# Performance work log

Measured on AMD Instinct MI355X. Metric: run time of the kernel, lower is better.

## Reference

```python
import jax, jax.numpy as jnp
from jax import lax
import numpy as np

B, S, I, H, L, D = 64, 1024, 512, 512, 2, 2  # batch, seq, input, hidden, layers, directions


def setup_inputs() -> dict:
    key = jax.random.key(0)
    ks = jax.random.split(key, 6)
    scale = 0.05  # keep gates out of saturation (torch code uses raw randn; scaled for numerics)
    return {
        "x": jax.random.normal(ks[0], (B, S, I), jnp.float32),
        "Wi": jax.random.normal(ks[1], (L, D, 3, I, H), jnp.float32) * scale,  # gates: [r, z, n]
        "Wh": jax.random.normal(ks[2], (L, D, 3, H, H), jnp.float32) * scale,
        "b": jax.random.normal(ks[3], (L, D, 3, H), jnp.float32) * scale,
        "fc_w": jax.random.normal(ks[4], (D * H, H), jnp.float32) * scale,
        "fc_b": jax.random.normal(ks[5], (H,), jnp.float32) * scale,
    }


def _run_layer(x_seq, wi, wh, bb):
    """One GRU layer, one direction. x_seq: [B,S,Hin]; wi/wh: [3,Hin,H]; bb: [3,H]."""
    batch = x_seq.shape[0]
    h_dim = wh.shape[-1]
    # Precompute all input projections (+biases) once: [S, 3, B, H]
    xs = jnp.einsum('bsi,gih->sgbh', x_seq, wi) + bb[None, :, None, :]

    def step(h, xg):
        r = jax.nn.sigmoid(xg[0] + h @ wh[0])
        z = jax.nn.sigmoid(xg[1] + h @ wh[1])
        n = jnp.tanh(xg[2] + r * (h @ wh[2]))
        h_next = (1.0 - z) * n + z * h
        return h_next, h_next

    h0 = jnp.zeros((batch, h_dim), x_seq.dtype)
    _, ys = lax.scan(step, h0, xs)  # ys: [S, B, H]
    return ys.transpose(1, 0, 2)  # [B, S, H]


def reference(x, Wi, Wh, b, fc_w, fc_b):
    n_layers = Wi.shape[0]
    # forward direction: stack layers, feed layer output as next layer input
    out_f = x
    for l in range(n_layers):
        out_f = _run_layer(out_f, Wi[l, 0], Wh[l, 0], b[l, 0])
    # backward direction: process time-reversed sequence, then flip back
    out_b = x[:, ::-1, :]
    for l in range(n_layers):
        out_b = _run_layer(out_b, Wi[l, 1], Wh[l, 1], b[l, 1])
    out_b = out_b[:, ::-1, :]
    outputs = jnp.concatenate([out_f, out_b], axis=2)  # [B, S, 2H]
    return outputs[:, -1, :] @ fc_w + fc_b  # [B, H]
```

## Files before the change

kernel.cpp:

```cpp
#include <hip/hip_runtime.h>
#include <cstdint>
#include <cmath>


typedef __attribute__((ext_vector_type(8))) short bf16x8;
typedef __attribute__((ext_vector_type(4))) float f32x4;
typedef __attribute__((ext_vector_type(4))) unsigned int u32x4;

#define DEV static __device__ __forceinline__

DEV unsigned short f2bf(float f) {
  union { float f; uint32_t u; } v; v.f = f;
  uint32_t u = v.u;
  return (unsigned short)((u + (((u >> 16) & 1u) + 0x7fffu)) >> 16);
}
DEV float bf2f(unsigned short h) {
  union { uint32_t u; float f; } v; v.u = ((uint32_t)h) << 16;
  return v.f;
}
DEV float fsig(float x)  { return 1.f / (1.f + __expf(-x)); }
DEV float ftanh(float x) { return 2.f / (1.f + __expf(-2.f * x)) - 1.f; }

static constexpr int Ss = 1024, Ii = 512;

static constexpr size_t WIMG_PER_LS = 131072;
static constexpr size_t OFF_WIMG = 0;
static constexpr size_t WIMG_BYTES = (size_t)64 * WIMG_PER_LS;
static constexpr size_t OFF_H1  = OFF_WIMG + WIMG_BYTES;
static constexpr size_t OFF_H2  = OFF_H1 + 524288;
static constexpr size_t OFF_FLG = OFF_H2 + 524288;
static constexpr size_t OFF_H2F = OFF_FLG + 1024;
static constexpr size_t OFF_HB1 = OFF_H2F + 131072;
static constexpr size_t OFF_HB2 = OFF_HB1 + 131072;
static constexpr size_t WS_NEED = OFF_HB2 + 131072;

__global__ __launch_bounds__(256) void prep_weights(const float* __restrict__ Wi,
                                                    const float* __restrict__ Wh,
                                                    unsigned short* __restrict__ img) {
  uint32_t idx = blockIdx.x * 256 + threadIdx.x;
  uint32_t ls = idx >> 16;
  uint32_t off = idx & 65535u;
  int l = (int)(ls >> 5), s = (int)(ls & 31);
  int m, g, cc, kg, kr;
  bool lo = off >= 49152u;
  if (!lo) {
    m = (int)(off / 24576u); uint32_t r = off % 24576u;
    kg = (int)(r / 384u); r %= 384u;
    int c = (int)(r >> 3); kr = (int)(r & 7u);
    g = c >> 4; cc = c & 15;
  } else {
    uint32_t o2 = off - 49152u;
    m = (int)(o2 >> 13); uint32_t r = o2 & 8191u;
    kg = (int)(r >> 7); r &= 127u;
    cc = (int)(r >> 3); kr = (int)(r & 7u);
    g = 2;
  }
  int h = s * 16 + cc, k = kg * 8 + kr;
  const float* W = m ? Wh : Wi;
  float v = W[((size_t)(l * 6 + g) * 512 + k) * 512 + h];
  unsigned short hv = f2bf(v);
  if (lo) hv = f2bf(v - bf2f(hv));
  img[(size_t)ls * 65536 + off] = hv;
}

__global__ __launch_bounds__(256) void init_state(uint32_t* __restrict__ hz,
                                                  int* __restrict__ flg) {
  int tid = blockIdx.x * 256 + threadIdx.x;
  if (tid < 262144) hz[tid] = 0u;
  if (tid < 64) flg[tid] = (tid >= 32) ? 1 : 0;
}

#define MFMA(AA, BB, CC) CC = __builtin_amdgcn_mfma_f32_16x16x32_bf16(AA, BB, CC, 0, 0, 0)

#define WAIT2(TA, TB)                                                              \
  {                                                                                \
    const int tgt_ = (lane < 32) ? (TA) : (TB);                                    \
    int spins_ = 0;                                                                \
    for (;;) {                                                                     \
      int v_ = __hip_atomic_load(pollp, __ATOMIC_RELAXED, __HIP_MEMORY_SCOPE_AGENT); \
      if (__all(v_ >= tgt_)) break;                                                \
      __builtin_amdgcn_s_sleep(1);                                                 \
      if (++spins_ > (1 << 20)) {                                                  \
        __hip_atomic_fetch_max((int*)pollp, 0x40000000, __ATOMIC_RELAXED,          \
                               __HIP_MEMORY_SCOPE_AGENT);                          \
        break;                                                                     \
      }                                                                            \
    }                                                                              \
    __builtin_amdgcn_fence(__ATOMIC_ACQUIRE, "agent");                             \
  }

__global__ __launch_bounds__(256, 1) void gru_persistent(const float* __restrict__ x,
                                                         const float* __restrict__ bias,
                                                         unsigned char* __restrict__ ws) {
  __shared__ unsigned char lds[131072];
  const int tid = threadIdx.x, lane = tid & 63, wv = tid >> 6;
  const int bid = blockIdx.x;
  const int layer = bid >> 5, slice = bid & 31;
  const int l15 = lane & 15, q = lane >> 4;

  {
    const u32x4* src = (const u32x4*)(ws + OFF_WIMG + (size_t)(layer * 32 + slice) * WIMG_PER_LS);
    u32x4* dst = (u32x4*)lds;
    for (int i = tid; i < 8192; i += 256) dst[i] = src[i];
  }
  __syncthreads();

  bf16x8 hB[48];
#pragma unroll
  for (int kk = 0; kk < 16; ++kk) {
    const int kg = kk * 4 + q;
    const unsigned char* wb = lds + 49152 + (size_t)kg * 768 + (size_t)l15 * 16;
    hB[kk * 3 + 0] = *(const bf16x8*)(wb);
    hB[kk * 3 + 1] = *(const bf16x8*)(wb + 256);
    hB[kk * 3 + 2] = *(const bf16x8*)(wb + 512);
  }

  unsigned short* h1 = (unsigned short*)(ws + OFF_H1);
  unsigned short* h2 = (unsigned short*)(ws + OFF_H2);
  int* flg = (int*)(ws + OFF_FLG);
  float* h2f = (float*)(ws + OFF_H2F);

  const int colg = slice * 16 + l15;
  const int row0 = wv * 16 + q * 4;
  const float b0 = bias[(size_t)(layer * 6 + 0) * 512 + colg];
  const float b1 = bias[(size_t)(layer * 6 + 1) * 512 + colg];
  const float b2 = bias[(size_t)(layer * 6 + 2) * 512 + colg];

  int* myflag = flg + layer * 32 + slice;
  const int* pollp = flg + lane;
  f32x4 hprev{0.f, 0.f, 0.f, 0.f};

  if (layer == 0) {
    const float* xr0 = x + (size_t)(wv * 16 + l15) * Ss * Ii;
    for (int T = 1; T <= 1024; ++T) {
      f32x4 ax0{}, ax1{}, ax2{}, ah0{}, ah1{}, ah2{};
      const float* xr = xr0 + (size_t)(T - 1) * Ii;
#pragma unroll 4
      for (int kk = 0; kk < 16; ++kk) {
        const int kg = kk * 4 + q;
        f32x4 va = *(const f32x4*)(xr + kg * 8);
        f32x4 vb = *(const f32x4*)(xr + kg * 8 + 4);
        bf16x8 ahi, alo;
#pragma unroll
        for (int e = 0; e < 4; ++e) {
          unsigned short ha = f2bf(va[e]);
          ((unsigned short*)&ahi)[e] = ha;
          ((unsigned short*)&alo)[e] = f2bf(va[e] - bf2f(ha));
          unsigned short hb_ = f2bf(vb[e]);
          ((unsigned short*)&ahi)[e + 4] = hb_;
          ((unsigned short*)&alo)[e + 4] = f2bf(vb[e] - bf2f(hb_));
        }
        const unsigned char* wb = lds + (size_t)kg * 768 + (size_t)l15 * 16;
        bf16x8 q0 = *(const bf16x8*)(wb);
        bf16x8 q1 = *(const bf16x8*)(wb + 256);
        bf16x8 q2 = *(const bf16x8*)(wb + 512);
        bf16x8 ql = *(const bf16x8*)(lds + 98304 + (size_t)kg * 256 + (size_t)l15 * 16);
        MFMA(ahi, q0, ax0); MFMA(alo, q0, ax0);
        MFMA(ahi, q1, ax1); MFMA(alo, q1, ax1);
        MFMA(ahi, q2, ax2); MFMA(alo, q2, ax2);
        MFMA(ahi, ql, ax2);
      }
      WAIT2(T - 1, T - 3);
      const unsigned short* hsrc = h1 + (size_t)((T - 1) & 3) * 65536 + (size_t)(wv * 16 + l15) * 512;
#pragma unroll
      for (int kk = 0; kk < 16; ++kk) {
        const int kg = kk * 4 + q;
        bf16x8 ahi = *(const bf16x8*)(hsrc + kg * 8);
        bf16x8 alo = *(const bf16x8*)(hsrc + 32768 + kg * 8);
        bf16x8 ql = *(const bf16x8*)(lds + 98304 + 16384 + (size_t)kg * 256 + (size_t)l15 * 16);
        MFMA(ahi, hB[kk * 3 + 0], ah0); MFMA(alo, hB[kk * 3 + 0], ah0);
        MFMA(ahi, hB[kk * 3 + 1], ah1); MFMA(alo, hB[kk * 3 + 1], ah1);
        MFMA(ahi, hB[kk * 3 + 2], ah2); MFMA(alo, hB[kk * 3 + 2], ah2);
        MFMA(ahi, ql, ah2);
      }
      unsigned short* hd = h1 + (size_t)(T & 3) * 65536;
#pragma unroll
      for (int e = 0; e < 4; ++e) {
        float rr = fsig(ax0[e] + ah0[e] + b0);
        float zz = fsig(ax1[e] + ah1[e] + b1);
        float nn = ftanh(ax2[e] + b2 + rr * ah2[e]);
        float hn = (1.f - zz) * nn + zz * hprev[e];
        hprev[e] = hn;
        unsigned short hi = f2bf(hn), lo = f2bf(hn - bf2f(hi));
        size_t o = (size_t)(row0 + e) * 512 + colg;
        hd[o] = hi; hd[o + 32768] = lo;
      }
      __syncthreads();
      if (tid == 0)
        __hip_atomic_fetch_max(myflag, T, __ATOMIC_RELEASE, __HIP_MEMORY_SCOPE_AGENT);
    }
  } else {
    for (int T = 2; T <= 1025; ++T) {
      WAIT2(T - 1, T - 1);
      f32x4 ax0{}, ax1{}, ax2{}, ah0{}, ah1{}, ah2{};
      const unsigned short* as = h1 + (size_t)((T - 1) & 3) * 65536 + (size_t)(wv * 16 + l15) * 512;
      const unsigned short* hsrc = h2 + (size_t)((T - 2) & 3) * 65536 + (size_t)(wv * 16 + l15) * 512;
#pragma unroll 4
      for (int kk = 0; kk < 16; ++kk) {
        const int kg = kk * 4 + q;
        bf16x8 ahi = *(const bf16x8*)(as + kg * 8);
        bf16x8 alo = *(const bf16x8*)(as + 32768 + kg * 8);
        const unsigned char* wb = lds + (size_t)kg * 768 + (size_t)l15 * 16;
        bf16x8 q0 = *(const bf16x8*)(wb);
        bf16x8 q1 = *(const bf16x8*)(wb + 256);
        bf16x8 q2 = *(const bf16x8*)(wb + 512);
        bf16x8 ql = *(const bf16x8*)(lds + 98304 + (size_t)kg * 256 + (size_t)l15 * 16);
        MFMA(ahi, q0, ax0); MFMA(alo, q0, ax0);
        MFMA(ahi, q1, ax1); MFMA(alo, q1, ax1);
        MFMA(ahi, q2, ax2); MFMA(alo, q2, ax2);
        MFMA(ahi, ql, ax2);
      }
#pragma unroll
      for (int kk = 0; kk < 16; ++kk) {
        const int kg = kk * 4 + q;
        bf16x8 ahi = *(const bf16x8*)(hsrc + kg * 8);
        bf16x8 alo = *(const bf16x8*)(hsrc + 32768 + kg * 8);
        bf16x8 ql = *(const bf16x8*)(lds + 98304 + 16384 + (size_t)kg * 256 + (size_t)l15 * 16);
        MFMA(ahi, hB[kk * 3 + 0], ah0); MFMA(alo, hB[kk * 3 + 0], ah0);
        MFMA(ahi, hB[kk * 3 + 1], ah1); MFMA(alo, hB[kk * 3 + 1], ah1);
        MFMA(ahi, hB[kk * 3 + 2], ah2); MFMA(alo, hB[kk * 3 + 2], ah2);
        MFMA(ahi, ql, ah2);
      }
      unsigned short* hd = h2 + (size_t)((T - 1) & 3) * 65536;
#pragma unroll
      for (int e = 0; e < 4; ++e) {
        float rr = fsig(ax0[e] + ah0[e] + b0);
        float zz = fsig(ax1[e] + ah1[e] + b1);
        float nn = ftanh(ax2[e] + b2 + rr * ah2[e]);
        float hn = (1.f - zz) * nn + zz * hprev[e];
        hprev[e] = hn;
        unsigned short hi = f2bf(hn), lo = f2bf(hn - bf2f(hi));
        size_t o = (size_t)(row0 + e) * 512 + colg;
        hd[o] = hi; hd[o + 32768] = lo;
        if (T == 1025) h2f[o] = hn;
      }
      __syncthreads();
      if (tid == 0)
        __hip_atomic_fetch_max(myflag, T, __ATOMIC_RELEASE, __HIP_MEMORY_SCOPE_AGENT);
    }
  }
}

__global__ __launch_bounds__(256) void gru_bstep(const float* __restrict__ inp, long rstride,
                                                 const float* __restrict__ Wi,
                                                 const float* __restrict__ bias,
                                                 float* __restrict__ out) {
  __shared__ float a[8192];
  int tid = threadIdx.x;
  int bg = blockIdx.x >> 4, cg = blockIdx.x & 15;
  for (int j = 0; j < 32; ++j) {
    int idx = j * 256 + tid;
    int r = idx >> 9, k = idx & 511;
    a[idx] = inp[(size_t)(bg * 16 + r) * rstride + k];
  }
  __syncthreads();
  int col = cg * 32 + (tid & 31);
  int r0 = tid >> 5;
  float z0 = bias[512 + col], z1 = z0;
  float n0 = bias[1024 + col], n1 = n0;
  const float* W1 = Wi + (size_t)512 * 512;
  const float* W2 = Wi + (size_t)2 * 512 * 512;
  for (int k = 0; k < 512; ++k) {
    float wz = W1[(size_t)k * 512 + col];
    float wn = W2[(size_t)k * 512 + col];
    float a0 = a[r0 * 512 + k], a1 = a[(r0 + 8) * 512 + k];
    z0 += a0 * wz; z1 += a1 * wz;
    n0 += a0 * wn; n1 += a1 * wn;
  }
  float s0 = fsig(z0), s1 = fsig(z1);
  out[(size_t)(bg * 16 + r0) * 512 + col]     = (1.f - s0) * ftanh(n0);
  out[(size_t)(bg * 16 + r0 + 8) * 512 + col] = (1.f - s1) * ftanh(n1);
}

__global__ __launch_bounds__(256) void fc_kernel(const float* __restrict__ h2f,
                                                 const float* __restrict__ hb2,
                                                 const float* __restrict__ fcw,
                                                 const float* __restrict__ fcb,
                                                 float* __restrict__ out) {
  __shared__ float a[16384];
  int tid = threadIdx.x;
  int bg = blockIdx.x >> 4, cg = blockIdx.x & 15;
  for (int j = 0; j < 32; ++j) {
    int idx = j * 256 + tid;
    int r = idx >> 9, k = idx & 511;
    a[r * 1024 + k]       = h2f[(size_t)(bg * 16 + r) * 512 + k];
    a[r * 1024 + 512 + k] = hb2[(size_t)(bg * 16 + r) * 512 + k];
  }
  __syncthreads();
  int col = cg * 32 + (tid & 31);
  int r0 = tid >> 5;
  float s0 = fcb[col], s1 = fcb[col];
  for (int k = 0; k < 1024; ++k) {
    float wvv = fcw[(size_t)k * 512 + col];
    s0 += a[r0 * 1024 + k] * wvv;
    s1 += a[(r0 + 8) * 1024 + k] * wvv;
  }
  out[(size_t)(bg * 16 + r0) * 512 + col]     = s0;
  out[(size_t)(bg * 16 + r0 + 8) * 512 + col] = s1;
}

extern "C" void kernel_launch(void* const* d_in, const int* in_sizes, int n_in,
                              void* d_out, int out_size, void* d_ws, size_t ws_size,
                              hipStream_t stream) {
  const float* x   = (const float*)d_in[0];
  const float* Wi  = (const float*)d_in[1];
  const float* Wh  = (const float*)d_in[2];
  const float* b   = (const float*)d_in[3];
  const float* fcw = (const float*)d_in[4];
  const float* fcb = (const float*)d_in[5];
  float* out = (float*)d_out;
  unsigned char* ws = (unsigned char*)d_ws;
  if (ws_size < WS_NEED) return;

  prep_weights<<<16384, 256, 0, stream>>>(Wi, Wh, (unsigned short*)(ws + OFF_WIMG));
  init_state<<<1024, 256, 0, stream>>>((uint32_t*)(ws + OFF_H1), (int*)(ws + OFF_FLG));
  gru_persistent<<<64, 256, 0, stream>>>(x, b, ws);
  gru_bstep<<<64, 256, 0, stream>>>(x + (size_t)1023 * 512, (long)Ss * Ii,
                                    Wi + (size_t)3 * 512 * 512, b + 3 * 512,
                                    (float*)(ws + OFF_HB1));
  gru_bstep<<<64, 256, 0, stream>>>((const float*)(ws + OFF_HB1), 512L,
                                    Wi + (size_t)9 * 512 * 512, b + 9 * 512,
                                    (float*)(ws + OFF_HB2));
  fc_kernel<<<64, 256, 0, stream>>>((const float*)(ws + OFF_H2F), (const float*)(ws + OFF_HB2),
                                    fcw, fcb, out);
}
```

Measured before the change: 15.37 ms.

## Replace acquire/release flag sync with relaxed atomics and split per-layer waits

The inter-block handshake now uses relaxed agent-scope atomic loads and stores for the h state buffers and an explicit vmcnt wait, in place of acquire fences and release flag updates. This avoids cache invalidation and writeback costs on each step. Waits are split per producer group, so layer 1 can start its own recurrent matmul before layer 0's output is ready, and layer 0 checks the consumer's progress before starting its input projection. The correctness of the relaxed ordering depends on the atomic accesses bypassing non-coherent caches, which is a memory-model risk.

```diff
diff --git a/kernel.cpp b/kernel.cpp
--- a/kernel.cpp
+++ b/kernel.cpp
@@ -72,22 +72,30 @@
 
 #define MFMA(AA, BB, CC) CC = __builtin_amdgcn_mfma_f32_16x16x32_bf16(AA, BB, CC, 0, 0, 0)
 
-#define WAIT2(TA, TB)                                                              \
-  {                                                                                \
-    const int tgt_ = (lane < 32) ? (TA) : (TB);                                    \
-    int spins_ = 0;                                                                \
-    for (;;) {                                                                     \
-      int v_ = __hip_atomic_load(pollp, __ATOMIC_RELAXED, __HIP_MEMORY_SCOPE_AGENT); \
-      if (__all(v_ >= tgt_)) break;                                                \
-      __builtin_amdgcn_s_sleep(1);                                                 \
-      if (++spins_ > (1 << 20)) {                                                  \
-        __hip_atomic_fetch_max((int*)pollp, 0x40000000, __ATOMIC_RELAXED,          \
-                               __HIP_MEMORY_SCOPE_AGENT);                          \
-        break;                                                                     \
-      }                                                                            \
-    }                                                                              \
-    __builtin_amdgcn_fence(__ATOMIC_ACQUIRE, "agent");                             \
-  }
+DEV bf16x8 ldc16(const unsigned short* p) {
+  union { unsigned long long q[2]; bf16x8 v; } u;
+  u.q[0] = __hip_atomic_load((const unsigned long long*)p,       __ATOMIC_RELAXED, __HIP_MEMORY_SCOPE_AGENT);
+  u.q[1] = __hip_atomic_load((const unsigned long long*)(p + 4), __ATOMIC_RELAXED, __HIP_MEMORY_SCOPE_AGENT);
+  return u.v;
+}
+DEV void stc16(unsigned short* p, unsigned short v) {
+  __hip_atomic_store(p, v, __ATOMIC_RELAXED, __HIP_MEMORY_SCOPE_AGENT);
+}
+
+DEV void waitflag(int* flg, int grp, int tgt, int lane) {
+  int* p = flg + grp * 32 + (lane & 31);
+  int spins = 0;
+  for (;;) {
+    int v = __hip_atomic_load(p, __ATOMIC_RELAXED, __HIP_MEMORY_SCOPE_AGENT);
+    if (__all(v >= tgt)) break;
+    __builtin_amdgcn_s_sleep(2);
+    if (++spins > (1 << 19)) {
+      __hip_atomic_fetch_max(p, 0x40000000, __ATOMIC_RELAXED, __HIP_MEMORY_SCOPE_AGENT);
+      break;
+    }
+  }
+  asm volatile("" ::: "memory");
+}
 
 __global__ __launch_bounds__(256, 1) void gru_persistent(const float* __restrict__ x,
                                                          const float* __restrict__ bias,
@@ -127,12 +135,12 @@
   const float b2 = bias[(size_t)(layer * 6 + 2) * 512 + colg];
 
   int* myflag = flg + layer * 32 + slice;
-  const int* pollp = flg + lane;
   f32x4 hprev{0.f, 0.f, 0.f, 0.f};
 
   if (layer == 0) {
     const float* xr0 = x + (size_t)(wv * 16 + l15) * Ss * Ii;
     for (int T = 1; T <= 1024; ++T) {
+      waitflag(flg, 1, T - 3, lane);
       f32x4 ax0{}, ax1{}, ax2{}, ah0{}, ah1{}, ah2{};
       const float* xr = xr0 + (size_t)(T - 1) * Ii;
 #pragma unroll 4
@@ -160,13 +168,13 @@
         MFMA(ahi, q2, ax2); MFMA(alo, q2, ax2);
         MFMA(ahi, ql, ax2);
       }
-      WAIT2(T - 1, T - 3);
+      waitflag(flg, 0, T - 1, lane);
       const unsigned short* hsrc = h1 + (size_t)((T - 1) & 3) * 65536 + (size_t)(wv * 16 + l15) * 512;
 #pragma unroll
       for (int kk = 0; kk < 16; ++kk) {
         const int kg = kk * 4 + q;
-        bf16x8 ahi = *(const bf16x8*)(hsrc + kg * 8);
-        bf16x8 alo = *(const bf16x8*)(hsrc + 32768 + kg * 8);
+        bf16x8 ahi = ldc16(hsrc + kg * 8);
+        bf16x8 alo = ldc16(hsrc + 32768 + kg * 8);
         bf16x8 ql = *(const bf16x8*)(lds + 98304 + 16384 + (size_t)kg * 256 + (size_t)l15 * 16);
         MFMA(ahi, hB[kk * 3 + 0], ah0); MFMA(alo, hB[kk * 3 + 0], ah0);
         MFMA(ahi, hB[kk * 3 + 1], ah1); MFMA(alo, hB[kk * 3 + 1], ah1);
@@ -183,23 +191,36 @@
         hprev[e] = hn;
         unsigned short hi = f2bf(hn), lo = f2bf(hn - bf2f(hi));
         size_t o = (size_t)(row0 + e) * 512 + colg;
-        hd[o] = hi; hd[o + 32768] = lo;
-      }
+        stc16(hd + o, hi); stc16(hd + o + 32768, lo);
+      }
+      asm volatile("s_waitcnt vmcnt(0)" ::: "memory");
       __syncthreads();
       if (tid == 0)
-        __hip_atomic_fetch_max(myflag, T, __ATOMIC_RELEASE, __HIP_MEMORY_SCOPE_AGENT);
+        __hip_atomic_fetch_max(myflag, T, __ATOMIC_RELAXED, __HIP_MEMORY_SCOPE_AGENT);
     }
   } else {
     for (int T = 2; T <= 1025; ++T) {
-      WAIT2(T - 1, T - 1);
       f32x4 ax0{}, ax1{}, ax2{}, ah0{}, ah1{}, ah2{};
+      waitflag(flg, 1, T - 1, lane);
+      const unsigned short* hsrc = h2 + (size_t)((T - 2) & 3) * 65536 + (size_t)(wv * 16 + l15) * 512;
+#pragma unroll
+      for (int kk = 0; kk < 16; ++kk) {
+        const int kg = kk * 4 + q;
+        bf16x8 ahi = ldc16(hsrc + kg * 8);
+        bf16x8 alo = ldc16(hsrc + 32768 + kg * 8);
+        bf16x8 ql = *(const bf16x8*)(lds + 98304 + 16384 + (size_t)kg * 256 + (size_t)l15 * 16);
+        MFMA(ahi, hB[kk * 3 + 0], ah0); MFMA(alo, hB[kk * 3 + 0], ah0);
+        MFMA(ahi, hB[kk * 3 + 1], ah1); MFMA(alo, hB[kk * 3 + 1], ah1);
+        MFMA(ahi, hB[kk * 3 + 2], ah2); MFMA(alo, hB[kk * 3 + 2], ah2);
+        MFMA(ahi, ql, ah2);
+      }
+      waitflag(flg, 0, T - 1, lane);
       const unsigned short* as = h1 + (size_t)((T - 1) & 3) * 65536 + (size_t)(wv * 16 + l15) * 512;
-      const unsigned short* hsrc = h2 + (size_t)((T - 2) & 3) * 65536 + (size_t)(wv * 16 + l15) * 512;
 #pragma unroll 4
       for (int kk = 0; kk < 16; ++kk) {
         const int kg = kk * 4 + q;
-        bf16x8 ahi = *(const bf16x8*)(as + kg * 8);
-        bf16x8 alo = *(const bf16x8*)(as + 32768 + kg * 8);
+        bf16x8 ahi = ldc16(as + kg * 8);
+        bf16x8 alo = ldc16(as + 32768 + kg * 8);
         const unsigned char* wb = lds + (size_t)kg * 768 + (size_t)l15 * 16;
         bf16x8 q0 = *(const bf16x8*)(wb);
         bf16x8 q1 = *(const bf16x8*)(wb + 256);
@@ -210,17 +231,6 @@
         MFMA(ahi, q2, ax2); MFMA(alo, q2, ax2);
         MFMA(ahi, ql, ax2);
       }
-#pragma unroll
-      for (int kk = 0; kk < 16; ++kk) {
-        const int kg = kk * 4 + q;
-        bf16x8 ahi = *(const bf16x8*)(hsrc + kg * 8);
-        bf16x8 alo = *(const bf16x8*)(hsrc + 32768 + kg * 8);
-        bf16x8 ql = *(const bf16x8*)(lds + 98304 + 16384 + (size_t)kg * 256 + (size_t)l15 * 16);
-        MFMA(ahi, hB[kk * 3 + 0], ah0); MFMA(alo, hB[kk * 3 + 0], ah0);
-        MFMA(ahi, hB[kk * 3 + 1], ah1); MFMA(alo, hB[kk * 3 + 1], ah1);
-        MFMA(ahi, hB[kk * 3 + 2], ah2); MFMA(alo, hB[kk * 3 + 2], ah2);
-        MFMA(ahi, ql, ah2);
-      }
       unsigned short* hd = h2 + (size_t)((T - 1) & 3) * 65536;
 #pragma unroll
       for (int e = 0; e < 4; ++e) {
@@ -231,12 +241,13 @@
         hprev[e] = hn;
         unsigned short hi = f2bf(hn), lo = f2bf(hn - bf2f(hi));
         size_t o = (size_t)(row0 + e) * 512 + colg;
-        hd[o] = hi; hd[o + 32768] = lo;
+        stc16(hd + o, hi); stc16(hd + o + 32768, lo);
         if (T == 1025) h2f[o] = hn;
       }
+      asm volatile("s_waitcnt vmcnt(0)" ::: "memory");
       __syncthreads();
       if (tid == 0)
-        __hip_atomic_fetch_max(myflag, T, __ATOMIC_RELEASE, __HIP_MEMORY_SCOPE_AGENT);
+        __hip_atomic_fetch_max(myflag, T, __ATOMIC_RELAXED, __HIP_MEMORY_SCOPE_AGENT);
     }
   }
 }
```

Result: slower. 17.11 ms (+11.4%).

## Pad sync flags, map layers to XCDs, poll with one wave

Applied to the files above, without the earlier changes.

Each per-block progress flag now sits on its own 64-byte line (stride 16 ints) to avoid false sharing. Blocks are remapped so that each layer's slices land on particular XCDs (bid&7), keeping producer and consumer traffic local. Only wave 0 spins on the flags, with a longer sleep, and a __syncthreads releases the other waves. In layer 1 the recurrent h2 matmul is reordered ahead of the h1 input matmul. The trade-off is an extra block barrier per step and coarser polling latency.

```diff
diff --git a/kernel.cpp b/kernel.cpp
--- a/kernel.cpp
+++ b/kernel.cpp
@@ -29,7 +29,7 @@
 static constexpr size_t OFF_H1  = OFF_WIMG + WIMG_BYTES;
 static constexpr size_t OFF_H2  = OFF_H1 + 524288;
 static constexpr size_t OFF_FLG = OFF_H2 + 524288;
-static constexpr size_t OFF_H2F = OFF_FLG + 1024;
+static constexpr size_t OFF_H2F = OFF_FLG + 4096;
 static constexpr size_t OFF_HB1 = OFF_H2F + 131072;
 static constexpr size_t OFF_HB2 = OFF_HB1 + 131072;
 static constexpr size_t WS_NEED = OFF_HB2 + 131072;
@@ -67,27 +67,25 @@
                                                   int* __restrict__ flg) {
   int tid = blockIdx.x * 256 + threadIdx.x;
   if (tid < 262144) hz[tid] = 0u;
-  if (tid < 64) flg[tid] = (tid >= 32) ? 1 : 0;
+  if (tid < 1024) flg[tid] = ((tid & 15) == 0 && tid >= 512) ? 1 : 0;
 }
 
 #define MFMA(AA, BB, CC) CC = __builtin_amdgcn_mfma_f32_16x16x32_bf16(AA, BB, CC, 0, 0, 0)
 
-#define WAIT2(TA, TB)                                                              \
-  {                                                                                \
-    const int tgt_ = (lane < 32) ? (TA) : (TB);                                    \
-    int spins_ = 0;                                                                \
-    for (;;) {                                                                     \
-      int v_ = __hip_atomic_load(pollp, __ATOMIC_RELAXED, __HIP_MEMORY_SCOPE_AGENT); \
-      if (__all(v_ >= tgt_)) break;                                                \
-      __builtin_amdgcn_s_sleep(1);                                                 \
-      if (++spins_ > (1 << 20)) {                                                  \
-        __hip_atomic_fetch_max((int*)pollp, 0x40000000, __ATOMIC_RELAXED,          \
-                               __HIP_MEMORY_SCOPE_AGENT);                          \
-        break;                                                                     \
-      }                                                                            \
-    }                                                                              \
-    __builtin_amdgcn_fence(__ATOMIC_ACQUIRE, "agent");                             \
-  }
+DEV void wait_combined(int* flg, int tgtA, int tgtB, int lane) {
+  int* p = flg + lane * 16;
+  const int tgt = (lane < 32) ? tgtA : tgtB;
+  int spins = 0;
+  for (;;) {
+    int v = __hip_atomic_load(p, __ATOMIC_RELAXED, __HIP_MEMORY_SCOPE_AGENT);
+    if (__all(v >= tgt)) break;
+    __builtin_amdgcn_s_sleep(4);
+    if (++spins > (1 << 17)) {
+      __hip_atomic_fetch_max(p, 0x40000000, __ATOMIC_RELAXED, __HIP_MEMORY_SCOPE_AGENT);
+      break;
+    }
+  }
+}
 
 __global__ __launch_bounds__(256, 1) void gru_persistent(const float* __restrict__ x,
                                                          const float* __restrict__ bias,
@@ -95,7 +93,9 @@
   __shared__ unsigned char lds[131072];
   const int tid = threadIdx.x, lane = tid & 63, wv = tid >> 6;
   const int bid = blockIdx.x;
-  const int layer = bid >> 5, slice = bid & 31;
+  const int xcd = bid & 7;
+  const int layer = xcd >> 2;
+  const int slice = (xcd & 3) * 8 + (bid >> 3);
   const int l15 = lane & 15, q = lane >> 4;
 
   {
@@ -126,8 +126,7 @@
   const float b1 = bias[(size_t)(layer * 6 + 1) * 512 + colg];
   const float b2 = bias[(size_t)(layer * 6 + 2) * 512 + colg];
 
-  int* myflag = flg + layer * 32 + slice;
-  const int* pollp = flg + lane;
+  int* myflag = flg + (layer * 32 + slice) * 16;
   f32x4 hprev{0.f, 0.f, 0.f, 0.f};
 
   if (layer == 0) {
@@ -160,7 +159,11 @@
         MFMA(ahi, q2, ax2); MFMA(alo, q2, ax2);
         MFMA(ahi, ql, ax2);
       }
-      WAIT2(T - 1, T - 3);
+      if (wv == 0) {
+        wait_combined(flg, T - 1, T - 3, lane);
+        __builtin_amdgcn_fence(__ATOMIC_ACQUIRE, "agent");
+      }
+      __syncthreads();
       const unsigned short* hsrc = h1 + (size_t)((T - 1) & 3) * 65536 + (size_t)(wv * 16 + l15) * 512;
 #pragma unroll
       for (int kk = 0; kk < 16; ++kk) {
@@ -191,10 +194,25 @@
     }
   } else {
     for (int T = 2; T <= 1025; ++T) {
-      WAIT2(T - 1, T - 1);
+      if (wv == 0) {
+        wait_combined(flg, T - 1, T - 1, lane);
+        __builtin_amdgcn_fence(__ATOMIC_ACQUIRE, "agent");
+      }
+      __syncthreads();
       f32x4 ax0{}, ax1{}, ax2{}, ah0{}, ah1{}, ah2{};
+      const unsigned short* hsrc = h2 + (size_t)((T - 2) & 3) * 65536 + (size_t)(wv * 16 + l15) * 512;
+#pragma unroll
+      for (int kk = 0; kk < 16; ++kk) {
+        const int kg = kk * 4 + q;
+        bf16x8 ahi = *(const bf16x8*)(hsrc + kg * 8);
+        bf16x8 alo = *(const bf16x8*)(hsrc + 32768 + kg * 8);
+        bf16x8 ql = *(const bf16x8*)(lds + 98304 + 16384 + (size_t)kg * 256 + (size_t)l15 * 16);
+        MFMA(ahi, hB[kk * 3 + 0], ah0); MFMA(alo, hB[kk * 3 + 0], ah0);
+        MFMA(ahi, hB[kk * 3 + 1], ah1); MFMA(alo, hB[kk * 3 + 1], ah1);
+        MFMA(ahi, hB[kk * 3 + 2], ah2); MFMA(alo, hB[kk * 3 + 2], ah2);
+        MFMA(ahi, ql, ah2);
+      }
       const unsigned short* as = h1 + (size_t)((T - 1) & 3) * 65536 + (size_t)(wv * 16 + l15) * 512;
-      const unsigned short* hsrc = h2 + (size_t)((T - 2) & 3) * 65536 + (size_t)(wv * 16 + l15) * 512;
 #pragma unroll 4
       for (int kk = 0; kk < 16; ++kk) {
         const int kg = kk * 4 + q;
@@ -210,17 +228,6 @@
         MFMA(ahi, q2, ax2); MFMA(alo, q2, ax2);
         MFMA(ahi, ql, ax2);
       }
-#pragma unroll
-      for (int kk = 0; kk < 16; ++kk) {
-        const int kg = kk * 4 + q;
-        bf16x8 ahi = *(const bf16x8*)(hsrc + kg * 8);
-        bf16x8 alo = *(const bf16x8*)(hsrc + 32768 + kg * 8);
-        bf16x8 ql = *(const bf16x8*)(lds + 98304 + 16384 + (size_t)kg * 256 + (size_t)l15 * 16);
-        MFMA(ahi, hB[kk * 3 + 0], ah0); MFMA(alo, hB[kk * 3 + 0], ah0);
-        MFMA(ahi, hB[kk * 3 + 1], ah1); MFMA(alo, hB[kk * 3 + 1], ah1);
-        MFMA(ahi, hB[kk * 3 + 2], ah2); MFMA(alo, hB[kk * 3 + 2], ah2);
-        MFMA(ahi, ql, ah2);
-      }
       unsigned short* hd = h2 + (size_t)((T - 1) & 3) * 65536;
 #pragma unroll
       for (int e = 0; e < 4; ++e) {
```

After: 15.22 ms. No clear change (-1.0%).

## Replace persistent spin-wait GRU kernel with per-timestep kernel launches

Applied to the files above, without the earlier changes.

Drops the persistent kernel that kept each slice's weights in LDS and registers and synchronized layers through global atomic flags with spin-waiting. Instead it launches one kernel per timestep (1025 launches), with layer 1 at T and layer 2 at T-1 running in the same launch, and relies on stream ordering for synchronization. Weights are now read from global memory every step, and the previous hidden state is reloaded from the global buffer. This removes the polling overhead and deadlock risk, but adds launch overhead and repeated weight traffic each step.

```diff
diff --git a/kernel.cpp b/kernel.cpp
--- a/kernel.cpp
+++ b/kernel.cpp
@@ -28,8 +28,7 @@
 static constexpr size_t WIMG_BYTES = (size_t)64 * WIMG_PER_LS;
 static constexpr size_t OFF_H1  = OFF_WIMG + WIMG_BYTES;
 static constexpr size_t OFF_H2  = OFF_H1 + 524288;
-static constexpr size_t OFF_FLG = OFF_H2 + 524288;
-static constexpr size_t OFF_H2F = OFF_FLG + 1024;
+static constexpr size_t OFF_H2F = OFF_H2 + 524288;
 static constexpr size_t OFF_HB1 = OFF_H2F + 131072;
 static constexpr size_t OFF_HB2 = OFF_HB1 + 131072;
 static constexpr size_t WS_NEED = OFF_HB2 + 131072;
@@ -63,180 +62,137 @@
   img[(size_t)ls * 65536 + off] = hv;
 }
 
-__global__ __launch_bounds__(256) void init_state(uint32_t* __restrict__ hz,
-                                                  int* __restrict__ flg) {
+__global__ __launch_bounds__(256) void init_state(uint32_t* __restrict__ hz) {
   int tid = blockIdx.x * 256 + threadIdx.x;
   if (tid < 262144) hz[tid] = 0u;
-  if (tid < 64) flg[tid] = (tid >= 32) ? 1 : 0;
 }
 
 #define MFMA(AA, BB, CC) CC = __builtin_amdgcn_mfma_f32_16x16x32_bf16(AA, BB, CC, 0, 0, 0)
 
-#define WAIT2(TA, TB)                                                              \
-  {                                                                                \
-    const int tgt_ = (lane < 32) ? (TA) : (TB);                                    \
-    int spins_ = 0;                                                                \
-    for (;;) {                                                                     \
-      int v_ = __hip_atomic_load(pollp, __ATOMIC_RELAXED, __HIP_MEMORY_SCOPE_AGENT); \
-      if (__all(v_ >= tgt_)) break;                                                \
-      __builtin_amdgcn_s_sleep(1);                                                 \
-      if (++spins_ > (1 << 20)) {                                                  \
-        __hip_atomic_fetch_max((int*)pollp, 0x40000000, __ATOMIC_RELAXED,          \
-                               __HIP_MEMORY_SCOPE_AGENT);                          \
-        break;                                                                     \
-      }                                                                            \
-    }                                                                              \
-    __builtin_amdgcn_fence(__ATOMIC_ACQUIRE, "agent");                             \
-  }
-
-__global__ __launch_bounds__(256, 1) void gru_persistent(const float* __restrict__ x,
-                                                         const float* __restrict__ bias,
-                                                         unsigned char* __restrict__ ws) {
-  __shared__ unsigned char lds[131072];
+__global__ __launch_bounds__(256) void gru_step(const float* __restrict__ x,
+                                                const float* __restrict__ bias,
+                                                unsigned char* __restrict__ ws,
+                                                int T) {
   const int tid = threadIdx.x, lane = tid & 63, wv = tid >> 6;
   const int bid = blockIdx.x;
-  const int layer = bid >> 5, slice = bid & 31;
+  const int isL2 = bid >> 5;
+  const int slice = bid & 31;
   const int l15 = lane & 15, q = lane >> 4;
-
-  {
-    const u32x4* src = (const u32x4*)(ws + OFF_WIMG + (size_t)(layer * 32 + slice) * WIMG_PER_LS);
-    u32x4* dst = (u32x4*)lds;
-    for (int i = tid; i < 8192; i += 256) dst[i] = src[i];
-  }
-  __syncthreads();
-
-  bf16x8 hB[48];
-#pragma unroll
-  for (int kk = 0; kk < 16; ++kk) {
-    const int kg = kk * 4 + q;
-    const unsigned char* wb = lds + 49152 + (size_t)kg * 768 + (size_t)l15 * 16;
-    hB[kk * 3 + 0] = *(const bf16x8*)(wb);
-    hB[kk * 3 + 1] = *(const bf16x8*)(wb + 256);
-    hB[kk * 3 + 2] = *(const bf16x8*)(wb + 512);
-  }
-
-  unsigned short* h1 = (unsigned short*)(ws + OFF_H1);
-  unsigned short* h2 = (unsigned short*)(ws + OFF_H2);
-  int* flg = (int*)(ws + OFF_FLG);
-  float* h2f = (float*)(ws + OFF_H2F);
+  if (!isL2 && T > 1024) return;
+  if (isL2 && T < 2) return;
+
+  const unsigned short* img = (const unsigned short*)(ws + OFF_WIMG) + (size_t)(isL2 * 32 + slice) * 65536;
+  unsigned char* h1b = ws + OFF_H1;
+  unsigned char* h2b = ws + OFF_H2;
 
   const int colg = slice * 16 + l15;
   const int row0 = wv * 16 + q * 4;
-  const float b0 = bias[(size_t)(layer * 6 + 0) * 512 + colg];
-  const float b1 = bias[(size_t)(layer * 6 + 1) * 512 + colg];
-  const float b2 = bias[(size_t)(layer * 6 + 2) * 512 + colg];
-
-  int* myflag = flg + layer * 32 + slice;
-  const int* pollp = flg + lane;
-  f32x4 hprev{0.f, 0.f, 0.f, 0.f};
-
-  if (layer == 0) {
-    const float* xr0 = x + (size_t)(wv * 16 + l15) * Ss * Ii;
-    for (int T = 1; T <= 1024; ++T) {
-      f32x4 ax0{}, ax1{}, ax2{}, ah0{}, ah1{}, ah2{};
-      const float* xr = xr0 + (size_t)(T - 1) * Ii;
+  const int arow = wv * 16 + l15;
+  const float b0 = bias[(size_t)(isL2 * 6 + 0) * 512 + colg];
+  const float b1 = bias[(size_t)(isL2 * 6 + 1) * 512 + colg];
+  const float b2 = bias[(size_t)(isL2 * 6 + 2) * 512 + colg];
+
+  f32x4 ax0{}, ax1{}, ax2{}, ah0{}, ah1{}, ah2{};
+
+  if (!isL2) {
+    const float* xr = x + (size_t)arow * Ss * Ii + (size_t)(T - 1) * Ii;
+    const unsigned char* hp = h1b + (size_t)((T - 1) & 3) * 131072;
+    const unsigned char* hpa = hp + (size_t)arow * 1024;
 #pragma unroll 4
-      for (int kk = 0; kk < 16; ++kk) {
-        const int kg = kk * 4 + q;
-        f32x4 va = *(const f32x4*)(xr + kg * 8);
-        f32x4 vb = *(const f32x4*)(xr + kg * 8 + 4);
-        bf16x8 ahi, alo;
-#pragma unroll
-        for (int e = 0; e < 4; ++e) {
-          unsigned short ha = f2bf(va[e]);
-          ((unsigned short*)&ahi)[e] = ha;
-          ((unsigned short*)&alo)[e] = f2bf(va[e] - bf2f(ha));
-          unsigned short hb_ = f2bf(vb[e]);
-          ((unsigned short*)&ahi)[e + 4] = hb_;
-          ((unsigned short*)&alo)[e + 4] = f2bf(vb[e] - bf2f(hb_));
-        }
-        const unsigned char* wb = lds + (size_t)kg * 768 + (size_t)l15 * 16;
-        bf16x8 q0 = *(const bf16x8*)(wb);
-        bf16x8 q1 = *(const bf16x8*)(wb + 256);
-        bf16x8 q2 = *(const bf16x8*)(wb + 512);
-        bf16x8 ql = *(const bf16x8*)(lds + 98304 + (size_t)kg * 256 + (size_t)l15 * 16);
-        MFMA(ahi, q0, ax0); MFMA(alo, q0, ax0);
-        MFMA(ahi, q1, ax1); MFMA(alo, q1, ax1);
-        MFMA(ahi, q2, ax2); MFMA(alo, q2, ax2);
-        MFMA(ahi, ql, ax2);
-      }
-      WAIT2(T - 1, T - 3);
-      const unsigned short* hsrc = h1 + (size_t)((T - 1) & 3) * 65536 + (size_t)(wv * 16 + l15) * 512;
-#pragma unroll
-      for (int kk = 0; kk < 16; ++kk) {
-        const int kg = kk * 4 + q;
-        bf16x8 ahi = *(const bf16x8*)(hsrc + kg * 8);
-        bf16x8 alo = *(const bf16x8*)(hsrc + 32768 + kg * 8);
-        bf16x8 ql = *(const bf16x8*)(lds + 98304 + 16384 + (size_t)kg * 256 + (size_t)l15 * 16);
-        MFMA(ahi, hB[kk * 3 + 0], ah0); MFMA(alo, hB[kk * 3 + 0], ah0);
-        MFMA(ahi, hB[kk * 3 + 1], ah1); MFMA(alo, hB[kk * 3 + 1], ah1);
-        MFMA(ahi, hB[kk * 3 + 2], ah2); MFMA(alo, hB[kk * 3 + 2], ah2);
-        MFMA(ahi, ql, ah2);
-      }
-      unsigned short* hd = h1 + (size_t)(T & 3) * 65536;
+    for (int kk = 0; kk < 16; ++kk) {
+      const int kg = kk * 4 + q;
+      f32x4 va = *(const f32x4*)(xr + kg * 8);
+      f32x4 vb = *(const f32x4*)(xr + kg * 8 + 4);
+      bf16x8 xhi, xlo;
 #pragma unroll
       for (int e = 0; e < 4; ++e) {
-        float rr = fsig(ax0[e] + ah0[e] + b0);
-        float zz = fsig(ax1[e] + ah1[e] + b1);
-        float nn = ftanh(ax2[e] + b2 + rr * ah2[e]);
-        float hn = (1.f - zz) * nn + zz * hprev[e];
-        hprev[e] = hn;
-        unsigned short hi = f2bf(hn), lo = f2bf(hn - bf2f(hi));
-        size_t o = (size_t)(row0 + e) * 512 + colg;
-        hd[o] = hi; hd[o + 32768] = lo;
+        unsigned short ha = f2bf(va[e]);
+        ((unsigned short*)&xhi)[e] = ha;
+        ((unsigned short*)&xlo)[e] = f2bf(va[e] - bf2f(ha));
+        unsigned short hb_ = f2bf(vb[e]);
+        ((unsigned short*)&xhi)[e + 4] = hb_;
+        ((unsigned short*)&xlo)[e + 4] = f2bf(vb[e] - bf2f(hb_));
       }
-      __syncthreads();
-      if (tid == 0)
-        __hip_atomic_fetch_max(myflag, T, __ATOMIC_RELEASE, __HIP_MEMORY_SCOPE_AGENT);
+      bf16x8 hhi = *(const bf16x8*)(hpa + (size_t)kg * 16);
+      bf16x8 hlo = *(const bf16x8*)(hpa + (size_t)kg * 16 + 65536);
+      const unsigned short* wi = img + (size_t)kg * 384 + l15 * 8;
+      const unsigned short* wh = img + 24576 + (size_t)kg * 384 + l15 * 8;
+      bf16x8 i0 = *(const bf16x8*)(wi);
+      bf16x8 i1 = *(const bf16x8*)(wi + 128);
+      bf16x8 i2 = *(const bf16x8*)(wi + 256);
+      bf16x8 il = *(const bf16x8*)(img + 49152 + (size_t)kg * 128 + l15 * 8);
+      bf16x8 w0 = *(const bf16x8*)(wh);
+      bf16x8 w1 = *(const bf16x8*)(wh + 128);
+      bf16x8 w2 = *(const bf16x8*)(wh + 256);
+      bf16x8 wl = *(const bf16x8*)(img + 57344 + (size_t)kg * 128 + l15 * 8);
+      MFMA(xhi, i0, ax0); MFMA(xlo, i0, ax0);
+      MFMA(xhi, i1, ax1); MFMA(xlo, i1, ax1);
+      MFMA(xhi, i2, ax2); MFMA(xlo, i2, ax2);
+      MFMA(xhi, il, ax2);
+      MFMA(hhi, w0, ah0); MFMA(hlo, w0, ah0);
+      MFMA(hhi, w1, ah1); MFMA(hlo, w1, ah1);
+      MFMA(hhi, w2, ah2); MFMA(hlo, w2, ah2);
+      MFMA(hhi, wl, ah2);
+    }
+    unsigned char* hd = h1b + (size_t)(T & 3) * 131072;
+#pragma unroll
+    for (int e = 0; e < 4; ++e) {
+      size_t ob = (size_t)(row0 + e) * 1024 + (size_t)colg * 2;
+      float hprev = bf2f(*(const unsigned short*)(hp + ob)) +
+                    bf2f(*(const unsigned short*)(hp + ob + 65536));
+      float rr = fsig(ax0[e] + ah0[e] + b0);
+      float zz = fsig(ax1[e] + ah1[e] + b1);
+      float nn = ftanh(ax2[e] + b2 + rr * ah2[e]);
+      float hn = (1.f - zz) * nn + zz * hprev;
+      unsigned short hi = f2bf(hn), lo = f2bf(hn - bf2f(hi));
+      *(unsigned short*)(hd + ob) = hi;
+      *(unsigned short*)(hd + ob + 65536) = lo;
     }
   } else {
-    for (int T = 2; T <= 1025; ++T) {
-      WAIT2(T - 1, T - 1);
-      f32x4 ax0{}, ax1{}, ax2{}, ah0{}, ah1{}, ah2{};
-      const unsigned short* as = h1 + (size_t)((T - 1) & 3) * 65536 + (size_t)(wv * 16 + l15) * 512;
-      const unsigned short* hsrc = h2 + (size_t)((T - 2) & 3) * 65536 + (size_t)(wv * 16 + l15) * 512;
+    const unsigned char* ap1 = h1b + (size_t)((T - 1) & 3) * 131072 + (size_t)arow * 1024;
+    const unsigned char* hp2 = h2b + (size_t)((T - 2) & 3) * 131072;
+    const unsigned char* ap2 = hp2 + (size_t)arow * 1024;
 #pragma unroll 4
-      for (int kk = 0; kk < 16; ++kk) {
-        const int kg = kk * 4 + q;
-        bf16x8 ahi = *(const bf16x8*)(as + kg * 8);
-        bf16x8 alo = *(const bf16x8*)(as + 32768 + kg * 8);
-        const unsigned char* wb = lds + (size_t)kg * 768 + (size_t)l15 * 16;
-        bf16x8 q0 = *(const bf16x8*)(wb);
-        bf16x8 q1 = *(const bf16x8*)(wb + 256);
-        bf16x8 q2 = *(const bf16x8*)(wb + 512);
-        bf16x8 ql = *(const bf16x8*)(lds + 98304 + (size_t)kg * 256 + (size_t)l15 * 16);
-        MFMA(ahi, q0, ax0); MFMA(alo, q0, ax0);
-        MFMA(ahi, q1, ax1); MFMA(alo, q1, ax1);
-        MFMA(ahi, q2, ax2); MFMA(alo, q2, ax2);
-        MFMA(ahi, ql, ax2);
-      }
+    for (int kk = 0; kk < 16; ++kk) {
+      const int kg = kk * 4 + q;
+      bf16x8 a1h = *(const bf16x8*)(ap1 + (size_t)kg * 16);
+      bf16x8 a1l = *(const bf16x8*)(ap1 + (size_t)kg * 16 + 65536);
+      bf16x8 a2h = *(const bf16x8*)(ap2 + (size_t)kg * 16);
+      bf16x8 a2l = *(const bf16x8*)(ap2 + (size_t)kg * 16 + 65536);
+      const unsigned short* wi = img + (size_t)kg * 384 + l15 * 8;
+      const unsigned short* wh = img + 24576 + (size_t)kg * 384 + l15 * 8;
+      bf16x8 i0 = *(const bf16x8*)(wi);
+      bf16x8 i1 = *(const bf16x8*)(wi + 128);
+      bf16x8 i2 = *(const bf16x8*)(wi + 256);
+      bf16x8 il = *(const bf16x8*)(img + 49152 + (size_t)kg * 128 + l15 * 8);
+      bf16x8 w0 = *(const bf16x8*)(wh);
+      bf16x8 w1 = *(const bf16x8*)(wh + 128);
+      bf16x8 w2 = *(const bf16x8*)(wh + 256);
+      bf16x8 wl = *(const bf16x8*)(img + 57344 + (size_t)kg * 128 + l15 * 8);
+      MFMA(a1h, i0, ax0); MFMA(a1l, i0, ax0);
+      MFMA(a1h, i1, ax1); MFMA(a1l, i1, ax1);
+      MFMA(a1h, i2, ax2); MFMA(a1l, i2, ax2);
+      MFMA(a1h, il, ax2);
+      MFMA(a2h, w0, ah0); MFMA(a2l, w0, ah0);
+      MFMA(a2h, w1, ah1); MFMA(a2l, w1, ah1);
+      MFMA(a2h, w2, ah2); MFMA(a2l, w2, ah2);
+      MFMA(a2h, wl, ah2);
+    }
+    unsigned char* hd = h2b + (size_t)((T - 1) & 3) * 131072;
+    float* h2f = (float*)(ws + OFF_H2F);
 #pragma unroll
-      for (int kk = 0; kk < 16; ++kk) {
-        const int kg = kk * 4 + q;
-        bf16x8 ahi = *(const bf16x8*)(hsrc + kg * 8);
-        bf16x8 alo = *(const bf16x8*)(hsrc + 32768 + kg * 8);
-        bf16x8 ql = *(const bf16x8*)(lds + 98304 + 16384 + (size_t)kg * 256 + (size_t)l15 * 16);
-        MFMA(ahi, hB[kk * 3 + 0], ah0); MFMA(alo, hB[kk * 3 + 0], ah0);
-        MFMA(ahi, hB[kk * 3 + 1], ah1); MFMA(alo, hB[kk * 3 + 1], ah1);
-        MFMA(ahi, hB[kk * 3 + 2], ah2); MFMA(alo, hB[kk * 3 + 2], ah2);
-        MFMA(ahi, ql, ah2);
-      }
-      unsigned short* hd = h2 + (size_t)((T - 1) & 3) * 65536;
-#pragma unroll
-      for (int e = 0; e < 4; ++e) {
-        float rr = fsig(ax0[e] + ah0[e] + b0);
-        float zz = fsig(ax1[e] + ah1[e] + b1);
-        float nn = ftanh(ax2[e] + b2 + rr * ah2[e]);
-        float hn = (1.f - zz) * nn + zz * hprev[e];
-        hprev[e] = hn;
-        unsigned short hi = f2bf(hn), lo = f2bf(hn - bf2f(hi));
-        size_t o = (size_t)(row0 + e) * 512 + colg;
-        hd[o] = hi; hd[o + 32768] = lo;
-        if (T == 1025) h2f[o] = hn;
-      }
-      __syncthreads();
-      if (tid == 0)
-        __hip_atomic_fetch_max(myflag, T, __ATOMIC_RELEASE, __HIP_MEMORY_SCOPE_AGENT);
+    for (int e = 0; e < 4; ++e) {
+      size_t ob = (size_t)(row0 + e) * 1024 + (size_t)colg * 2;
+      float hprev = bf2f(*(const unsigned short*)(hp2 + ob)) +
+                    bf2f(*(const unsigned short*)(hp2 + ob + 65536));
+      float rr = fsig(ax0[e] + ah0[e] + b0);
+      float zz = fsig(ax1[e] + ah1[e] + b1);
+      float nn = ftanh(ax2[e] + b2 + rr * ah2[e]);
+      float hn = (1.f - zz) * nn + zz * hprev;
+      unsigned short hi = f2bf(hn), lo = f2bf(hn - bf2f(hi));
+      *(unsigned short*)(hd + ob) = hi;
+      *(unsigned short*)(hd + ob + 65536) = lo;
+      if (T == 1025) h2f[(size_t)(row0 + e) * 512 + colg] = hn;
     }
   }
 }
@@ -313,8 +269,9 @@
   if (ws_size < WS_NEED) return;
 
   prep_weights<<<16384, 256, 0, stream>>>(Wi, Wh, (unsigned short*)(ws + OFF_WIMG));
-  init_state<<<1024, 256, 0, stream>>>((uint32_t*)(ws + OFF_H1), (int*)(ws + OFF_FLG));
-  gru_persistent<<<64, 256, 0, stream>>>(x, b, ws);
+  init_state<<<1024, 256, 0, stream>>>((uint32_t*)(ws + OFF_H1));
+  for (int T = 1; T <= 1025; ++T)
+    gru_step<<<64, 256, 0, stream>>>(x, b, ws, T);
   gru_bstep<<<64, 256, 0, stream>>>(x + (size_t)1023 * 512, (long)Ss * Ii,
                                     Wi + (size_t)3 * 512 * 512, b + 3 * 512,
                                     (float*)(ws + OFF_HB1));
```

Result: slower. 16.78 ms (+9.2%).
